# Kernel optimization log

Measured on AMD Instinct MI355X. Metric: run time of the kernel, lower is better.

The kernel has to match this reference:

```python
import jax, jax.numpy as jnp
import numpy as np

NUM_HEADS = 12
KSIZE = 3
PAD = 1


def setup_inputs() -> dict:
    key = jax.random.key(0)
    ks = jax.random.split(key, 5)
    B, H, W, C = 4, 96, 96, 192
    x = jax.random.normal(ks[0], (B, H * W, C), jnp.float32)
    Wq = jax.random.normal(ks[1], (W, W), jnp.float32) * 0.02
    bq = jnp.zeros((W,), jnp.float32)
    Wkv = jax.random.normal(ks[2], (2 * W, W), jnp.float32) * 0.02
    bkv = jnp.zeros((2 * W,), jnp.float32)
    Wp = jax.random.normal(ks[3], (C, C), jnp.float32) * 0.02
    bp = jnp.zeros((C,), jnp.float32)
    f_qr = jnp.float32(1.0)
    f_kr = jnp.float32(1.0)
    f_vr = jnp.float32(1.0)
    return {"x": x, "Wq": Wq, "bq": bq, "Wkv": Wkv, "bkv": bkv, "Wp": Wp,
            "bp": bp, "f_qr": f_qr, "f_kr": f_kr, "f_vr": f_vr, "H": H, "W": W}


def reference(x, Wq, bq, Wkv, bkv, Wp, bp, f_qr, f_kr, f_vr, H, W):
    B, N, C = x.shape
    nh = NUM_HEADS
    hc = C // nh
    scale = C ** (-0.5)
    # faithful to torch: raw reshape of (B, N, C) into (B, C, H, W)
    xn = x.reshape(B, C, H, W)
    # q_proj is Linear over the last (width) axis, size Hw == W
    q = jnp.einsum('bchw,vw->bchv', xn, Wq) + bq            # (B,C,H,W)
    q = q.reshape(B, H, W, nh, hc).transpose(0, 3, 1, 2, 4)  # (B,nh,H,W,hc)
    q = (q * scale * f_qr).reshape(B, nh, H * W, hc)         # (B,nh,L,hc)
    # kv_proj: Linear(W -> 2W) over last axis
    kv = jnp.einsum('bchw,vw->bchv', xn, Wkv) + bkv          # (B,C,H,2W)
    kv = kv.reshape(B, H, W, 2, nh, hc).transpose(3, 0, 4, 5, 1, 2)  # (2,B,nh,hc,H,W)
    kv = jnp.pad(kv, ((0, 0),) * 4 + ((PAD, PAD), (PAD, PAD)))       # zero-pad spatial
    # unfold: 3x3 sliding windows, stride 1 -> one window per pixel
    patches = jnp.stack([kv[..., i:i + H, j:j + W]
                         for i in range(KSIZE) for j in range(KSIZE)], axis=4)
    # (2,B,nh,hc,9,H,W) -> (2,B,nh,L,9,hc); kernel index = kh*3+kw matches nn.Unfold
    patches = patches.reshape(2, B, nh, hc, KSIZE * KSIZE, H * W).transpose(0, 1, 2, 5, 4, 3)
    k = patches[0] * f_kr                                    # (B,nh,L,9,hc)
    v = patches[1] * f_vr
    attn = jax.nn.softmax(jnp.einsum('bnlc,bnlkc->bnlk', q, k), axis=-1)  # (B,nh,L,9)
    out = jnp.einsum('bnlk,bnlkc->bnlc', attn, v)            # (B,nh,L,hc)
    out = out.transpose(0, 2, 1, 3).reshape(B, H, W, C)      # (B,H,W,C)
    out = jnp.einsum('bhwc,oc->bhwo', out, Wp) + bp          # proj Linear(dim,dim)
    return out.reshape(B, H * W, C)
```

## Files before the change

kernel.cpp:

```cpp
#include <hip/hip_runtime.h>

#define HW2   96
#define NH    12
#define LPIX  (HW2*HW2)
#define BATCH 4

typedef __attribute__((ext_vector_type(8))) short bf16x8;
typedef __attribute__((ext_vector_type(4))) float f32x4;

static __device__ __forceinline__ float bf2f(unsigned short u) {
  union { unsigned int i; float f; } v; v.i = ((unsigned int)u) << 16; return v.f;
}
static __device__ __forceinline__ unsigned short f2bf(float f) {
  union { float f; unsigned int i; } v; v.f = f;
  unsigned int r = v.i + 0x7FFF + ((v.i >> 16) & 1);
  return (unsigned short)(r >> 16);
}

__global__ __launch_bounds__(256) void cvt_w_kernel(
    const float* __restrict__ Wq, const float* __restrict__ Wkv,
    const float* __restrict__ Wp,
    unsigned short* __restrict__ wqb, unsigned short* __restrict__ wkvb,
    unsigned short* __restrict__ wpb) {
  int i = blockIdx.x * 256 + threadIdx.x;
  if (i < 9216)       wqb[i]          = f2bf(Wq[i]);
  else if (i < 27648) wkvb[i - 9216]  = f2bf(Wkv[i - 9216]);
  else if (i < 64512) wpb[i - 27648]  = f2bf(Wp[i - 27648]);
}

__global__ __launch_bounds__(256, 2) void qkv_gemm(
    const float* __restrict__ X,
    const unsigned short* __restrict__ wq, const unsigned short* __restrict__ wkv,
    const float* __restrict__ bq, const float* __restrict__ bkv,
    const float* __restrict__ fqr, const float* __restrict__ fkr,
    const float* __restrict__ fvr,
    unsigned short* __restrict__ Qb, unsigned short* __restrict__ KVb)
{
  __shared__ unsigned short lds[19456];
  unsigned short* xs  = lds;
  unsigned short* qo  = lds;
  unsigned short* kvo = lds + 6656;

  const int tid = threadIdx.x;
  const int r0  = blockIdx.x * 64;

  const float4* xsrc = (const float4*)(X + (size_t)r0 * 96);
  #pragma unroll
  for (int it = 0; it < 6; it++) {
    int c = tid + it * 256;
    float4 v = xsrc[c];
    int row = c / 24, col = (c % 24) * 4;
    ushort4 p;
    p.x = f2bf(v.x); p.y = f2bf(v.y); p.z = f2bf(v.z); p.w = f2bf(v.w);
    *(ushort4*)&xs[row * 120 + col] = p;
  }
  __syncthreads();

  const int lane = tid & 63, w = tid >> 6;
  const int col  = lane & 15;
  const int koff = (lane >> 4) * 8;
  const int arow = 16 * w + (lane & 15);
  const int rloc = 16 * w + 4 * (lane >> 4);

  bf16x8 af0 = *(const bf16x8*)&xs[arow * 120 + koff];
  bf16x8 af1 = *(const bf16x8*)&xs[arow * 120 + koff + 32];
  bf16x8 af2 = *(const bf16x8*)&xs[arow * 120 + koff + 64];
  __syncthreads();

  const float fqr0 = fqr[0] * 0.07216878364870322f;
  const float fkr0 = fkr[0], fvr0 = fvr[0];

  #pragma unroll
  for (int g = 0; g < 3; g++) {
    bf16x8 bw0[6], bw1[6], bw2[6];
    #pragma unroll
    for (int j = 0; j < 6; j++) {
      int nt = g * 6 + j;
      const unsigned short* wrow = (nt < 6)
          ? wq  + (size_t)(nt * 16 + col) * 96 + koff
          : wkv + (size_t)((nt - 6) * 16 + col) * 96 + koff;
      bw0[j] = *(const bf16x8*)(wrow);
      bw1[j] = *(const bf16x8*)(wrow + 32);
      bw2[j] = *(const bf16x8*)(wrow + 64);
    }
    asm volatile("" ::: "memory");

    #pragma unroll
    for (int j = 0; j < 6; j++) {
      int nt = g * 6 + j;
      f32x4 acc = {0.f, 0.f, 0.f, 0.f};
      acc = __builtin_amdgcn_mfma_f32_16x16x32_bf16(af0, bw0[j], acc, 0, 0, 0);
      acc = __builtin_amdgcn_mfma_f32_16x16x32_bf16(af1, bw1[j], acc, 0, 0, 0);
      acc = __builtin_amdgcn_mfma_f32_16x16x32_bf16(af2, bw2[j], acc, 0, 0, 0);

      if (nt < 6) {
        int u = nt * 16 + col;
        float bias = bq[u];
        #pragma unroll
        for (int i = 0; i < 4; i++)
          qo[(rloc + i) * 104 + u] = f2bf((acc[i] + bias) * fqr0);
      } else {
        int u = (nt - 6) * 16 + col;
        float bias = bkv[u];
        #pragma unroll
        for (int i = 0; i < 4; i++) {
          float s = (i & 1) ? fvr0 : fkr0;
          kvo[(rloc + i) * 200 + u] = f2bf((acc[i] + bias) * s);
        }
      }
    }
  }
  __syncthreads();

  #pragma unroll
  for (int it = 0; it < 3; it++) {
    int c = tid + it * 256;
    int row = c / 12, cc = (c % 12) * 8;
    *(bf16x8*)(Qb + (size_t)(r0 + row) * 96 + cc) = *(const bf16x8*)&qo[row * 104 + cc];
  }
  #pragma unroll
  for (int it = 0; it < 6; it++) {
    int c = tid + it * 256;
    int row = c / 24, cc = (c % 24) * 8;
    *(bf16x8*)(KVb + (size_t)(r0 + row) * 192 + cc) = *(const bf16x8*)&kvo[row * 200 + cc];
  }
}

__global__ __launch_bounds__(384, 1) void attnproj_kernel(
    const unsigned short* __restrict__ Qb, const unsigned short* __restrict__ KVb,
    const unsigned short* __restrict__ wp, const float* __restrict__ bp,
    float* __restrict__ Out)
{
  __shared__ unsigned short s_out[32 * 204];
  const int tid = threadIdx.x;
  const int bid = (blockIdx.x & 7) * 144 + (blockIdx.x >> 3);
  const int bl0 = bid * 32;

  {
    const int n  = tid % NH;
    const int pl = tid / NH;
    const int bl = bl0 + pl;
    const int l  = bl % LPIX;
    const int b  = bl / LPIX;
    const int h2 = l / HW2, w2 = l - h2 * HW2;

    const unsigned short* qp = Qb + (size_t)bl * 192 + n * 16;
    uint4 qA = *(const uint4*)(qp);
    uint4 qB = *(const uint4*)(qp + 8);

    const unsigned short* kvb = KVb + (size_t)b * (LPIX * 384) + n * 16;

    int  nbo[9];
    bool okk[9];
    uint4 kA[9], kB[9], vA[9], vB[9];
    #pragma unroll
    for (int kk = 0; kk < 9; kk++) {
      int hh = h2 + kk / 3 - 1;
      int ww = w2 + kk % 3 - 1;
      okk[kk] = ((unsigned)hh < (unsigned)HW2) && ((unsigned)ww < (unsigned)HW2);
      int hc = min(max(hh, 0), HW2 - 1);
      int wc = min(max(ww, 0), HW2 - 1);
      nbo[kk] = (hc * HW2 + wc) * 384;
      const unsigned short* kp = kvb + nbo[kk];
      kA[kk] = *(const uint4*)(kp);
      kB[kk] = *(const uint4*)(kp + 8);
    }
    #pragma unroll
    for (int kk = 0; kk < 9; kk++) {
      const unsigned short* vp = kvb + nbo[kk] + 192;
      vA[kk] = *(const uint4*)(vp);
      vB[kk] = *(const uint4*)(vp + 8);
    }
    asm volatile("" ::: "memory");

    float q[16];
    {
      const unsigned short* qs = (const unsigned short*)&qA;
      #pragma unroll
      for (int j = 0; j < 8; j++) q[j] = bf2f(qs[j]);
      qs = (const unsigned short*)&qB;
      #pragma unroll
      for (int j = 0; j < 8; j++) q[8 + j] = bf2f(qs[j]);
    }

    float sc[9];
    #pragma unroll
    for (int kk = 0; kk < 9; kk++) {
      float s = 0.f;
      const unsigned short* kd = (const unsigned short*)&kA[kk];
      #pragma unroll
      for (int j = 0; j < 8; j++) s = fmaf(q[j], bf2f(kd[j]), s);
      kd = (const unsigned short*)&kB[kk];
      #pragma unroll
      for (int j = 0; j < 8; j++) s = fmaf(q[8 + j], bf2f(kd[j]), s);
      sc[kk] = okk[kk] ? s : 0.f;
    }

    float m = sc[0];
    #pragma unroll
    for (int kk = 1; kk < 9; kk++) m = fmaxf(m, sc[kk]);
    float ssum = 0.f;
    #pragma unroll
    for (int kk = 0; kk < 9; kk++) {
      float e = __expf(sc[kk] - m);
      sc[kk] = e;
      ssum += e;
    }

    float acc[16];
    #pragma unroll
    for (int j = 0; j < 16; j++) acc[j] = 0.f;
    #pragma unroll
    for (int kk = 0; kk < 9; kk++) {
      float wgt = okk[kk] ? sc[kk] : 0.f;
      const unsigned short* vd = (const unsigned short*)&vA[kk];
      #pragma unroll
      for (int j = 0; j < 8; j++) acc[j] = fmaf(wgt, bf2f(vd[j]), acc[j]);
      vd = (const unsigned short*)&vB[kk];
      #pragma unroll
      for (int j = 0; j < 8; j++) acc[8 + j] = fmaf(wgt, bf2f(vd[j]), acc[8 + j]);
    }
    float rinv = 1.f / ssum;
    unsigned short od[16];
    #pragma unroll
    for (int j = 0; j < 16; j++) od[j] = f2bf(acc[j] * rinv);
    unsigned short* op = s_out + pl * 204 + n * 16;
    *(uint4*)(op)     = *(uint4*)&od[0];
    *(uint4*)(op + 8) = *(uint4*)&od[8];
  }
  __syncthreads();

  const int lane = tid & 63, w = tid >> 6;
  const int wr = w & 1, wh = w >> 1;
  const int col  = lane & 15;
  const int koff = (lane >> 4) * 8;
  const int arow = 16 * wr + (lane & 15);
  const int rbase = bl0 + 16 * wr + 4 * (lane >> 4);

  bf16x8 af[6];
  #pragma unroll
  for (int kt = 0; kt < 6; kt++)
    af[kt] = *(const bf16x8*)&s_out[arow * 204 + koff + kt * 32];

  bf16x8 bw[4][6];
  #pragma unroll
  for (int t4 = 0; t4 < 4; t4++) {
    int nt = wh * 4 + t4;
    const unsigned short* wrow = wp + (size_t)(nt * 16 + col) * 192 + koff;
    #pragma unroll
    for (int kt = 0; kt < 6; kt++)
      bw[t4][kt] = *(const bf16x8*)(wrow + kt * 32);
  }
  asm volatile("" ::: "memory");

  #pragma unroll
  for (int t4 = 0; t4 < 4; t4++) {
    int nt = wh * 4 + t4;
    f32x4 acc = {0.f, 0.f, 0.f, 0.f};
    #pragma unroll
    for (int kt = 0; kt < 6; kt++)
      acc = __builtin_amdgcn_mfma_f32_16x16x32_bf16(af[kt], bw[t4][kt], acc, 0, 0, 0);
    int u = nt * 16 + col;
    float bias = bp[u];
    #pragma unroll
    for (int i = 0; i < 4; i++)
      Out[(size_t)(rbase + i) * 192 + u] = acc[i] + bias;
  }
}

extern "C" void kernel_launch(void* const* d_in, const int* in_sizes, int n_in,
                              void* d_out, int out_size, void* d_ws, size_t ws_size,
                              hipStream_t stream) {
  const float* x   = (const float*)d_in[0];
  const float* Wq  = (const float*)d_in[1];
  const float* bq  = (const float*)d_in[2];
  const float* Wkv = (const float*)d_in[3];
  const float* bkv = (const float*)d_in[4];
  const float* Wp  = (const float*)d_in[5];
  const float* bp  = (const float*)d_in[6];
  const float* fqr = (const float*)d_in[7];
  const float* fkr = (const float*)d_in[8];
  const float* fvr = (const float*)d_in[9];

  char* ws = (char*)d_ws;
  unsigned short* Qb   = (unsigned short*)ws;
  unsigned short* KVb  = (unsigned short*)(ws + 14155776);
  unsigned short* wqb  = (unsigned short*)(ws + 42467328);
  unsigned short* wkvb = (unsigned short*)(ws + 42485760);
  unsigned short* wpb  = (unsigned short*)(ws + 42522624);

  cvt_w_kernel<<<dim3(252), dim3(256), 0, stream>>>(Wq, Wkv, Wp, wqb, wkvb, wpb);

  qkv_gemm<<<dim3(1152), dim3(256), 0, stream>>>(
      x, wqb, wkvb, bq, bkv, fqr, fkr, fvr, Qb, KVb);

  attnproj_kernel<<<dim3(1152), dim3(384), 0, stream>>>(
      Qb, KVb, wpb, bp, (float*)d_out);
}
```

Baseline: 73.51 us.

## Drop LDS staging in QKV GEMM, load A fragments and store outputs directly

The QKV projection kernel now loads each lane's A-operand fragment straight from global fp32 memory into registers and converts it there, with no LDS staging and no barriers. Results are written directly to global as scalar bf16 stores rather than through an LDS tile with vectorized copy-out. Weight prefetch groups shrink from 6 to 3 tiles and launch bounds rise to 4 blocks per SIMD to allow higher occupancy. The cost is uncoalesced 2-byte scattered global stores in place of 16-byte coalesced ones.

```diff
diff --git a/kernel.cpp b/kernel.cpp
--- a/kernel.cpp
+++ b/kernel.cpp
@@ -28,7 +28,7 @@
   else if (i < 64512) wpb[i - 27648]  = f2bf(Wp[i - 27648]);
 }
 
-__global__ __launch_bounds__(256, 2) void qkv_gemm(
+__global__ __launch_bounds__(256, 4) void qkv_gemm(
     const float* __restrict__ X,
     const unsigned short* __restrict__ wq, const unsigned short* __restrict__ wkv,
     const float* __restrict__ bq, const float* __restrict__ bkv,
@@ -36,46 +36,38 @@
     const float* __restrict__ fvr,
     unsigned short* __restrict__ Qb, unsigned short* __restrict__ KVb)
 {
-  __shared__ unsigned short lds[19456];
-  unsigned short* xs  = lds;
-  unsigned short* qo  = lds;
-  unsigned short* kvo = lds + 6656;
-
-  const int tid = threadIdx.x;
-  const int r0  = blockIdx.x * 64;
-
-  const float4* xsrc = (const float4*)(X + (size_t)r0 * 96);
-  #pragma unroll
-  for (int it = 0; it < 6; it++) {
-    int c = tid + it * 256;
-    float4 v = xsrc[c];
-    int row = c / 24, col = (c % 24) * 4;
-    ushort4 p;
-    p.x = f2bf(v.x); p.y = f2bf(v.y); p.z = f2bf(v.z); p.w = f2bf(v.w);
-    *(ushort4*)&xs[row * 120 + col] = p;
-  }
-  __syncthreads();
-
+  const int tid  = threadIdx.x;
+  const int r0   = blockIdx.x * 64;
   const int lane = tid & 63, w = tid >> 6;
   const int col  = lane & 15;
   const int koff = (lane >> 4) * 8;
-  const int arow = 16 * w + (lane & 15);
-  const int rloc = 16 * w + 4 * (lane >> 4);
-
-  bf16x8 af0 = *(const bf16x8*)&xs[arow * 120 + koff];
-  bf16x8 af1 = *(const bf16x8*)&xs[arow * 120 + koff + 32];
-  bf16x8 af2 = *(const bf16x8*)&xs[arow * 120 + koff + 64];
-  __syncthreads();
+  const int arow = r0 + 16 * w + (lane & 15);
+  const int rbase = r0 + 16 * w + 4 * (lane >> 4);
+
+  const float* xr = X + (size_t)arow * 96;
+  float xv[24];
+  *(float4*)&xv[0]  = *(const float4*)(xr + koff);
+  *(float4*)&xv[4]  = *(const float4*)(xr + koff + 4);
+  *(float4*)&xv[8]  = *(const float4*)(xr + koff + 32);
+  *(float4*)&xv[12] = *(const float4*)(xr + koff + 36);
+  *(float4*)&xv[16] = *(const float4*)(xr + koff + 64);
+  *(float4*)&xv[20] = *(const float4*)(xr + koff + 68);
+  unsigned short au[24];
+  #pragma unroll
+  for (int j = 0; j < 24; j++) au[j] = f2bf(xv[j]);
+  bf16x8 af0 = *(const bf16x8*)&au[0];
+  bf16x8 af1 = *(const bf16x8*)&au[8];
+  bf16x8 af2 = *(const bf16x8*)&au[16];
 
   const float fqr0 = fqr[0] * 0.07216878364870322f;
   const float fkr0 = fkr[0], fvr0 = fvr[0];
 
   #pragma unroll
-  for (int g = 0; g < 3; g++) {
-    bf16x8 bw0[6], bw1[6], bw2[6];
-    #pragma unroll
-    for (int j = 0; j < 6; j++) {
-      int nt = g * 6 + j;
+  for (int g = 0; g < 6; g++) {
+    bf16x8 bw0[3], bw1[3], bw2[3];
+    #pragma unroll
+    for (int j = 0; j < 3; j++) {
+      int nt = g * 3 + j;
       const unsigned short* wrow = (nt < 6)
           ? wq  + (size_t)(nt * 16 + col) * 96 + koff
           : wkv + (size_t)((nt - 6) * 16 + col) * 96 + koff;
@@ -86,8 +78,8 @@
     asm volatile("" ::: "memory");
 
     #pragma unroll
-    for (int j = 0; j < 6; j++) {
-      int nt = g * 6 + j;
+    for (int j = 0; j < 3; j++) {
+      int nt = g * 3 + j;
       f32x4 acc = {0.f, 0.f, 0.f, 0.f};
       acc = __builtin_amdgcn_mfma_f32_16x16x32_bf16(af0, bw0[j], acc, 0, 0, 0);
       acc = __builtin_amdgcn_mfma_f32_16x16x32_bf16(af1, bw1[j], acc, 0, 0, 0);
@@ -98,31 +90,17 @@
         float bias = bq[u];
         #pragma unroll
         for (int i = 0; i < 4; i++)
-          qo[(rloc + i) * 104 + u] = f2bf((acc[i] + bias) * fqr0);
+          Qb[(size_t)(rbase + i) * 96 + u] = f2bf((acc[i] + bias) * fqr0);
       } else {
         int u = (nt - 6) * 16 + col;
         float bias = bkv[u];
         #pragma unroll
         for (int i = 0; i < 4; i++) {
           float s = (i & 1) ? fvr0 : fkr0;
-          kvo[(rloc + i) * 200 + u] = f2bf((acc[i] + bias) * s);
+          KVb[(size_t)(rbase + i) * 192 + u] = f2bf((acc[i] + bias) * s);
         }
       }
     }
-  }
-  __syncthreads();
-
-  #pragma unroll
-  for (int it = 0; it < 3; it++) {
-    int c = tid + it * 256;
-    int row = c / 12, cc = (c % 12) * 8;
-    *(bf16x8*)(Qb + (size_t)(r0 + row) * 96 + cc) = *(const bf16x8*)&qo[row * 104 + cc];
-  }
-  #pragma unroll
-  for (int it = 0; it < 6; it++) {
-    int c = tid + it * 256;
-    int row = c / 24, cc = (c % 24) * 8;
-    *(bf16x8*)(KVb + (size_t)(r0 + row) * 192 + cc) = *(const bf16x8*)&kvo[row * 200 + cc];
   }
 }
 
```

Result: no change. 74.61 us (+1.5%).
